# Performance work log

Measured on AMD Instinct MI355X. Metric: run time of the kernel, lower is better.

Reference implementation:

```python
import jax, jax.numpy as jnp
import numpy as np

D_MODEL = 512
N_HEADS = 8
D_K = D_MODEL // N_HEADS
LN_EPS = 1e-5


def setup_inputs() -> dict:
    key = jax.random.key(0)
    ks = jax.random.split(key, 8)
    B, S, D = 2, 4096, D_MODEL
    # xavier_uniform bound for square [D, D] weight
    bound = float(np.sqrt(6.0 / (D + D)))
    x = jax.random.normal(ks[0], (B, S, D), dtype=jnp.float32)
    w_q = jax.random.uniform(ks[1], (D, D), jnp.float32, -bound, bound)
    w_k = jax.random.uniform(ks[2], (D, D), jnp.float32, -bound, bound)
    w_v = jax.random.uniform(ks[3], (D, D), jnp.float32, -bound, bound)
    # w_o: torch Linear default init (kaiming-uniform-ish); uniform is fine as data
    lim = float(1.0 / np.sqrt(D))
    w_o = jax.random.uniform(ks[4], (D, D), jnp.float32, -lim, lim)
    b_o = jax.random.uniform(ks[5], (D,), jnp.float32, -lim, lim)
    ln_gamma = jnp.ones((D,), jnp.float32)
    ln_beta = jnp.zeros((D,), jnp.float32)
    return {"x": x, "w_q": w_q, "w_k": w_k, "w_v": w_v,
            "w_o": w_o, "b_o": b_o, "ln_gamma": ln_gamma, "ln_beta": ln_beta}


def _layer_norm(x, gamma, beta):
    mu = jnp.mean(x, axis=-1, keepdims=True)
    var = jnp.mean(jnp.square(x - mu), axis=-1, keepdims=True)
    return (x - mu) * jax.lax.rsqrt(var + LN_EPS) * gamma + beta


def reference(x, w_q, w_k, w_v, w_o, b_o, ln_gamma, ln_beta):
    B, S, D = x.shape
    residual = x
    h = _layer_norm(x, ln_gamma, ln_beta)
    # torch Linear: y = h @ W.T ; reshape to [B, H, S, d_k]
    def proj(W):
        return (h @ W.T).reshape(B, S, N_HEADS, D_K).transpose(0, 2, 1, 3)
    Q, K, V = proj(w_q), proj(w_k), proj(w_v)
    scores = jnp.einsum('bhqd,bhkd->bhqk', Q, K) / jnp.sqrt(jnp.float32(D_K))
    attn = jax.nn.softmax(scores, axis=-1)  # dropout p=0 -> identity
    attended = jnp.einsum('bhqk,bhkd->bhqd', attn, V)
    attended = attended.transpose(0, 2, 1, 3).reshape(B, S, D)
    out = attended @ w_o.T + b_o
    return out + residual
```

## Files before the change

kernel.cpp:

```cpp
#include <hip/hip_runtime.h>
#include <hip/hip_bf16.h>
#include <stdint.h>


typedef __bf16 bf16;
typedef __attribute__((ext_vector_type(8))) __bf16 bf16x8;
typedef __attribute__((ext_vector_type(4))) __bf16 bf16x4;
typedef __attribute__((ext_vector_type(4))) float f32x4;
typedef __attribute__((ext_vector_type(4))) unsigned int u32x4;

#define LOG2E 1.44269504088896340736f
#define SW(row, grp) (((row) << 6) + ((((grp) ^ ((row) & 7))) << 3))

__device__ __forceinline__ unsigned int pkbf16(float lo, float hi) {
  return __builtin_amdgcn_perm(__builtin_bit_cast(unsigned int, hi),
                               __builtin_bit_cast(unsigned int, lo),
                               0x07060302u);
}

__global__ __launch_bounds__(256) void ln_kernel(
    const float* __restrict__ x, const float* __restrict__ gamma,
    const float* __restrict__ beta, bf16* __restrict__ h) {
  int wave = threadIdx.x >> 6, lane = threadIdx.x & 63;
  int row = blockIdx.x * 4 + wave;
  const float* xr = x + (size_t)row * 512 + lane * 8;
  f32x4 v0 = *(const f32x4*)xr;
  f32x4 v1 = *(const f32x4*)(xr + 4);
  float f[8], s = 0.f, s2 = 0.f;
#pragma unroll
  for (int i = 0; i < 4; ++i) { f[i] = v0[i]; f[4 + i] = v1[i]; }
#pragma unroll
  for (int i = 0; i < 8; ++i) { s += f[i]; s2 += f[i] * f[i]; }
#pragma unroll
  for (int off = 1; off < 64; off <<= 1) {
    s  += __shfl_xor(s, off, 64);
    s2 += __shfl_xor(s2, off, 64);
  }
  float mu  = s * (1.f / 512.f);
  float var = s2 * (1.f / 512.f) - mu * mu;
  float rstd = rsqrtf(var + 1e-5f);
  f32x4 g0 = *(const f32x4*)(gamma + lane * 8);
  f32x4 g1 = *(const f32x4*)(gamma + lane * 8 + 4);
  f32x4 b0 = *(const f32x4*)(beta + lane * 8);
  f32x4 b1 = *(const f32x4*)(beta + lane * 8 + 4);
  bf16x8 o;
#pragma unroll
  for (int i = 0; i < 4; ++i) {
    o[i]     = (bf16)((f[i]     - mu) * rstd * g0[i] + b0[i]);
    o[4 + i] = (bf16)((f[4 + i] - mu) * rstd * g1[i] + b1[i]);
  }
  *(bf16x8*)(h + (size_t)row * 512 + lane * 8) = o;
}

__global__ __launch_bounds__(256) void qkv_kernel(
    const bf16* __restrict__ h, const float* __restrict__ wq,
    const float* __restrict__ wk, const float* __restrict__ wv,
    bf16* __restrict__ Qg, bf16* __restrict__ Kg, bf16* __restrict__ Vtg) {
  __shared__ bf16 As[128 * 64];
  __shared__ bf16 Bs[128 * 64];
  int tid = threadIdx.x, wave = tid >> 6, lane = tid & 63;
  int wm = wave >> 1, wn = wave & 1, quad = lane >> 4, l15 = lane & 15;
  int mtile = blockIdx.x;
  int wsel = blockIdx.y >> 2;
  int nb = blockIdx.y & 3;
  const float* W = (wsel == 0) ? wq : (wsel == 1 ? wk : wv);
  const bf16*  Abase = h + (size_t)mtile * 128 * 512;
  const float* Bbase = W + (size_t)nb * 128 * 512;
  f32x4 acc[4][4];
#pragma unroll
  for (int i = 0; i < 4; ++i)
#pragma unroll
    for (int j = 0; j < 4; ++j) acc[i][j] = (f32x4){0.f, 0.f, 0.f, 0.f};

  int srow = tid >> 3, grp = tid & 7, scol = grp * 8;
  bf16x8 ar[4];
  f32x4 br0[4], br1[4];
#pragma unroll
  for (int k = 0; k < 4; ++k) {
    int rr = srow + k * 32;
    ar[k]  = *(const bf16x8*)(Abase + (size_t)rr * 512 + scol);
    br0[k] = *(const f32x4*)(Bbase + (size_t)rr * 512 + scol);
    br1[k] = *(const f32x4*)(Bbase + (size_t)rr * 512 + scol + 4);
  }
  for (int k0 = 0; k0 < 512; k0 += 64) {
#pragma unroll
    for (int k = 0; k < 4; ++k) {
      int rr = srow + k * 32;
      int w = SW(rr, grp);
      *(bf16x8*)(As + w) = ar[k];
      bf16x8 wb;
#pragma unroll
      for (int j = 0; j < 4; ++j) { wb[j] = (bf16)br0[k][j]; wb[4 + j] = (bf16)br1[k][j]; }
      *(bf16x8*)(Bs + w) = wb;
    }
    __syncthreads();
    if (k0 < 448) {
#pragma unroll
      for (int k = 0; k < 4; ++k) {
        int rr = srow + k * 32;
        ar[k]  = *(const bf16x8*)(Abase + (size_t)rr * 512 + k0 + 64 + scol);
        br0[k] = *(const f32x4*)(Bbase + (size_t)rr * 512 + k0 + 64 + scol);
        br1[k] = *(const f32x4*)(Bbase + (size_t)rr * 512 + k0 + 64 + scol + 4);
      }
    }
#pragma unroll
    for (int c = 0; c < 2; ++c) {
      bf16x8 af[4], bw[4];
#pragma unroll
      for (int mt = 0; mt < 4; ++mt)
        af[mt] = *(const bf16x8*)(As + SW(wm * 64 + mt * 16 + l15, c * 4 + quad));
#pragma unroll
      for (int nt = 0; nt < 4; ++nt)
        bw[nt] = *(const bf16x8*)(Bs + SW(wn * 64 + nt * 16 + l15, c * 4 + quad));
#pragma unroll
      for (int mt = 0; mt < 4; ++mt)
#pragma unroll
        for (int nt = 0; nt < 4; ++nt)
          acc[mt][nt] = __builtin_amdgcn_mfma_f32_16x16x32_bf16(
              bw[nt], af[mt], acc[mt][nt], 0, 0, 0);
    }
    __syncthreads();
  }
  float qscale = (wsel == 0) ? (0.125f * LOG2E) : 1.0f;
#pragma unroll
  for (int mt = 0; mt < 4; ++mt) {
    int m_g = mtile * 128 + wm * 64 + mt * 16 + l15;
    int b = m_g >> 12, s = m_g & 4095;
#pragma unroll
    for (int nt = 0; nt < 4; ++nt) {
      int n_g = nb * 128 + wn * 64 + nt * 16 + quad * 4;
      int head = n_g >> 6, d = n_g & 63;
      f32x4 a = acc[mt][nt];
      if (wsel < 2) {
        bf16* dst = (wsel == 0 ? Qg : Kg) +
                    ((size_t)((b * 8 + head) * 4096 + s)) * 64 + d;
        bf16x4 pk;
#pragma unroll
        for (int r = 0; r < 4; ++r) pk[r] = (bf16)(a[r] * qscale);
        *(bf16x4*)dst = pk;
      } else {
        bf16* dst = Vtg + ((size_t)((b * 8 + head) * 64 + d)) * 4096 + s;
#pragma unroll
        for (int r = 0; r < 4; ++r) dst[(size_t)r * 4096] = (bf16)a[r];
      }
    }
  }
}

__global__ __launch_bounds__(256, 2) void attn_kernel(
    const bf16* __restrict__ Qg, const bf16* __restrict__ Kg,
    const bf16* __restrict__ Vtg, bf16* __restrict__ Og) {
  __shared__ char smem[64 * 1024];
  bf16* KV = (bf16*)smem;
  float* OL = (float*)smem;
  float* Ll = (float*)(smem + 49152);

  int tid = threadIdx.x, wave = tid >> 6, lane = tid & 63;
  int quad = lane >> 4, l15 = lane & 15;
  int qgrp = wave & 1, khalf = wave >> 1;
  int lin = blockIdx.x;
  int bh = ((lin & 7) << 1) | ((lin >> 3) & 1);
  int q0 = (lin >> 4) * 128;
  int hi = bh & 7, bi = bh >> 3;
  const bf16* Kh  = Kg  + (size_t)bh * 4096 * 64;
  const bf16* Vth = Vtg + (size_t)bh * 64 * 4096;

  bf16x8 qf[4][2];
#pragma unroll
  for (int mt = 0; mt < 4; ++mt)
#pragma unroll
    for (int c = 0; c < 2; ++c)
      qf[mt][c] = *(const bf16x8*)(
          Qg + ((size_t)bh * 4096 + q0 + qgrp * 64 + mt * 16 + l15) * 64 +
          c * 32 + quad * 8);

  f32x4 o_acc[4][4], lacc[4];
#pragma unroll
  for (int mt = 0; mt < 4; ++mt) {
    lacc[mt] = (f32x4){0.f, 0.f, 0.f, 0.f};
#pragma unroll
    for (int nt = 0; nt < 4; ++nt) o_acc[mt][nt] = (f32x4){0.f, 0.f, 0.f, 0.f};
  }
  const u32x4 onesu = {0x3F803F80u, 0x3F803F80u, 0x3F803F80u, 0x3F803F80u};
  const bf16x8 ones8 = __builtin_bit_cast(bf16x8, onesu);

  bf16* sbase = KV + khalf * 8192 + (qgrp ? 4096 : 0);
  bf16x8 sr[8];
  int key0 = khalf * 2048;
#pragma unroll
  for (int i = 0; i < 8; ++i) {
    int e = i * 512 + lane * 8;
    sr[i] = qgrp
        ? *(const bf16x8*)(Vth + (size_t)(e >> 6) * 4096 + key0 + (e & 63))
        : *(const bf16x8*)(Kh + (size_t)key0 * 64 + e);
  }
#pragma unroll
  for (int i = 0; i < 8; ++i) {
    int e = i * 512 + lane * 8;
    *(bf16x8*)(sbase + SW(e >> 6, (e >> 3) & 7)) = sr[i];
  }
#pragma unroll
  for (int i = 0; i < 8; ++i) {
    int e = i * 512 + lane * 8;
    sr[i] = qgrp
        ? *(const bf16x8*)(Vth + (size_t)(e >> 6) * 4096 + key0 + 64 + (e & 63))
        : *(const bf16x8*)(Kh + (size_t)(key0 + 64) * 64 + e);
  }
  __syncthreads();

  for (int kt = 0; kt < 32; ++kt) {
    int cur = kt & 1, nxt = cur ^ 1;
    bf16* Ksw = KV + cur * 16384 + khalf * 8192;
    bf16* Vsw = Ksw + 4096;
    if (kt < 31) {
#pragma unroll
      for (int i = 0; i < 8; ++i) {
        int e = i * 512 + lane * 8;
        *(bf16x8*)(sbase + nxt * 16384 + SW(e >> 6, (e >> 3) & 7)) = sr[i];
      }
    }
    if (kt < 30) {
      int kbase = key0 + (kt + 2) * 64;
#pragma unroll
      for (int i = 0; i < 8; ++i) {
        int e = i * 512 + lane * 8;
        sr[i] = qgrp
            ? *(const bf16x8*)(Vth + (size_t)(e >> 6) * 4096 + kbase + (e & 63))
            : *(const bf16x8*)(Kh + (size_t)kbase * 64 + e);
      }
    }
    bf16x8 kf[8];
#pragma unroll
    for (int kb = 0; kb < 4; ++kb)
#pragma unroll
      for (int c = 0; c < 2; ++c)
        kf[kb * 2 + c] = *(const bf16x8*)(Ksw + SW(kb * 16 + l15, c * 4 + quad));
    bf16x8 vf8[2][4];
#pragma unroll
    for (int pr = 0; pr < 2; ++pr)
#pragma unroll
      for (int nt = 0; nt < 4; ++nt) {
        bf16x4 lo = *(const bf16x4*)(
            &Vsw[SW(nt * 16 + l15, (pr * 2) * 2 + (quad >> 1)) + (quad & 1) * 4]);
        bf16x4 hi4 = *(const bf16x4*)(
            &Vsw[SW(nt * 16 + l15, (pr * 2 + 1) * 2 + (quad >> 1)) + (quad & 1) * 4]);
        bf16x8 v;
#pragma unroll
        for (int j = 0; j < 4; ++j) { v[j] = lo[j]; v[4 + j] = hi4[j]; }
        vf8[pr][nt] = v;
      }
#pragma unroll
    for (int mt = 0; mt < 4; ++mt) {
      f32x4 st[4];
#pragma unroll
      for (int kb = 0; kb < 4; ++kb) st[kb] = (f32x4){0.f, 0.f, 0.f, 0.f};
#pragma unroll
      for (int c = 0; c < 2; ++c)
#pragma unroll
        for (int kb = 0; kb < 4; ++kb)
          st[kb] = __builtin_amdgcn_mfma_f32_16x16x32_bf16(
              kf[kb * 2 + c], qf[mt][c], st[kb], 0, 0, 0);
#pragma unroll
      for (int pr = 0; pr < 2; ++pr) {
        float ea[4], eb[4];
#pragma unroll
        for (int r = 0; r < 4; ++r) {
          ea[r] = __builtin_amdgcn_exp2f(st[pr * 2][r]);
          eb[r] = __builtin_amdgcn_exp2f(st[pr * 2 + 1][r]);
        }
        u32x4 pw = {pkbf16(ea[0], ea[1]), pkbf16(ea[2], ea[3]),
                    pkbf16(eb[0], eb[1]), pkbf16(eb[2], eb[3])};
        bf16x8 pk8 = __builtin_bit_cast(bf16x8, pw);
#pragma unroll
        for (int nt = 0; nt < 4; ++nt)
          o_acc[mt][nt] = __builtin_amdgcn_mfma_f32_16x16x32_bf16(
              vf8[pr][nt], pk8, o_acc[mt][nt], 0, 0, 0);
        lacc[mt] = __builtin_amdgcn_mfma_f32_16x16x32_bf16(
            ones8, pk8, lacc[mt], 0, 0, 0);
      }
    }
    __syncthreads();
  }
  if (khalf == 1) {
    float* dst = OL + qgrp * 4096;
#pragma unroll
    for (int mt = 0; mt < 4; ++mt) {
#pragma unroll
      for (int nt = 0; nt < 4; ++nt) {
        int row = mt * 16 + l15;
        int g = nt * 4 + quad;
        int gs = (g & 8) | ((g ^ row) & 7);
        *(f32x4*)(&dst[row * 64 + gs * 4]) = o_acc[mt][nt];
      }
      if (quad == 0) Ll[qgrp * 64 + mt * 16 + l15] = lacc[mt][0];
    }
  }
  __syncthreads();
  if (khalf == 0) {
    const float* src = OL + qgrp * 4096;
#pragma unroll
    for (int mt = 0; mt < 4; ++mt) {
      float lt = lacc[mt][0] + Ll[qgrp * 64 + mt * 16 + l15];
      float inv = 1.0f / lt;
      int q = q0 + qgrp * 64 + mt * 16 + l15;
#pragma unroll
      for (int nt = 0; nt < 4; ++nt) {
        int row = mt * 16 + l15;
        int g = nt * 4 + quad;
        int gs = (g & 8) | ((g ^ row) & 7);
        f32x4 o = *(const f32x4*)(&src[row * 64 + gs * 4]);
        bf16x4 pk;
#pragma unroll
        for (int r = 0; r < 4; ++r)
          pk[r] = (bf16)((o[r] + o_acc[mt][nt][r]) * inv);
        *(bf16x4*)(&Og[((size_t)bi * 4096 + q) * 512 + hi * 64 + nt * 16 +
                       quad * 4]) = pk;
      }
    }
  }
}

__global__ __launch_bounds__(256) void proj_kernel(
    const bf16* __restrict__ A, const float* __restrict__ Wo,
    const float* __restrict__ bo, const float* __restrict__ x,
    float* __restrict__ out) {
  __shared__ bf16 As[128 * 64];
  __shared__ bf16 Bs[128 * 64];
  int tid = threadIdx.x, wave = tid >> 6, lane = tid & 63;
  int wm = wave >> 1, wn = wave & 1, quad = lane >> 4, l15 = lane & 15;
  int mtile = blockIdx.x, nb = blockIdx.y;
  const bf16*  Abase = A + (size_t)mtile * 128 * 512;
  const float* Bbase = Wo + (size_t)nb * 128 * 512;
  f32x4 acc[4][4];
#pragma unroll
  for (int i = 0; i < 4; ++i)
#pragma unroll
    for (int j = 0; j < 4; ++j) acc[i][j] = (f32x4){0.f, 0.f, 0.f, 0.f};

  int srow = tid >> 3, grp = tid & 7, scol = grp * 8;
  bf16x8 ar[4];
  f32x4 br0[4], br1[4];
#pragma unroll
  for (int k = 0; k < 4; ++k) {
    int rr = srow + k * 32;
    ar[k]  = *(const bf16x8*)(Abase + (size_t)rr * 512 + scol);
    br0[k] = *(const f32x4*)(Bbase + (size_t)rr * 512 + scol);
    br1[k] = *(const f32x4*)(Bbase + (size_t)rr * 512 + scol + 4);
  }
  for (int k0 = 0; k0 < 512; k0 += 64) {
#pragma unroll
    for (int k = 0; k < 4; ++k) {
      int rr = srow + k * 32;
      int w = SW(rr, grp);
      *(bf16x8*)(As + w) = ar[k];
      bf16x8 wb;
#pragma unroll
      for (int j = 0; j < 4; ++j) { wb[j] = (bf16)br0[k][j]; wb[4 + j] = (bf16)br1[k][j]; }
      *(bf16x8*)(Bs + w) = wb;
    }
    __syncthreads();
    if (k0 < 448) {
#pragma unroll
      for (int k = 0; k < 4; ++k) {
        int rr = srow + k * 32;
        ar[k]  = *(const bf16x8*)(Abase + (size_t)rr * 512 + k0 + 64 + scol);
        br0[k] = *(const f32x4*)(Bbase + (size_t)rr * 512 + k0 + 64 + scol);
        br1[k] = *(const f32x4*)(Bbase + (size_t)rr * 512 + k0 + 64 + scol + 4);
      }
    }
#pragma unroll
    for (int c = 0; c < 2; ++c) {
      bf16x8 af[4], bw[4];
#pragma unroll
      for (int mt = 0; mt < 4; ++mt)
        af[mt] = *(const bf16x8*)(As + SW(wm * 64 + mt * 16 + l15, c * 4 + quad));
#pragma unroll
      for (int nt = 0; nt < 4; ++nt)
        bw[nt] = *(const bf16x8*)(Bs + SW(wn * 64 + nt * 16 + l15, c * 4 + quad));
#pragma unroll
      for (int mt = 0; mt < 4; ++mt)
#pragma unroll
        for (int nt = 0; nt < 4; ++nt)
          acc[mt][nt] = __builtin_amdgcn_mfma_f32_16x16x32_bf16(
              bw[nt], af[mt], acc[mt][nt], 0, 0, 0);
    }
    __syncthreads();
  }
#pragma unroll
  for (int mt = 0; mt < 4; ++mt) {
    int m_g = mtile * 128 + wm * 64 + mt * 16 + l15;
#pragma unroll
    for (int nt = 0; nt < 4; ++nt) {
      int n_g = nb * 128 + wn * 64 + nt * 16 + quad * 4;
      f32x4 a = acc[mt][nt];
      f32x4 xr = *(const f32x4*)(x + (size_t)m_g * 512 + n_g);
      f32x4 bb = *(const f32x4*)(bo + n_g);
      f32x4 o;
#pragma unroll
      for (int r = 0; r < 4; ++r)
        o[r] = a[r] + bb[r] + xr[r];
      *(f32x4*)(out + (size_t)m_g * 512 + n_g) = o;
    }
  }
}

extern "C" void kernel_launch(void* const* d_in, const int* in_sizes, int n_in,
                              void* d_out, int out_size, void* d_ws, size_t ws_size,
                              hipStream_t stream) {
  const float* x     = (const float*)d_in[0];
  const float* wq    = (const float*)d_in[1];
  const float* wk    = (const float*)d_in[2];
  const float* wv    = (const float*)d_in[3];
  const float* wo    = (const float*)d_in[4];
  const float* bo    = (const float*)d_in[5];
  const float* gamma = (const float*)d_in[6];
  const float* beta  = (const float*)d_in[7];
  float* out = (float*)d_out;
  char* ws = (char*)d_ws;
  const size_t SZ = (size_t)8192 * 512 * sizeof(bf16);
  bf16* h   = (bf16*)(ws);
  bf16* Ao  = (bf16*)(ws);
  bf16* Qg  = (bf16*)(ws + SZ);
  bf16* Kg  = (bf16*)(ws + 2 * SZ);
  bf16* Vtg = (bf16*)(ws + 3 * SZ);

  ln_kernel<<<2048, 256, 0, stream>>>(x, gamma, beta, h);
  qkv_kernel<<<dim3(64, 12), 256, 0, stream>>>(h, wq, wk, wv, Qg, Kg, Vtg);
  attn_kernel<<<512, 256, 0, stream>>>(Qg, Kg, Vtg, Ao);
  proj_kernel<<<dim3(64, 4), 256, 0, stream>>>(Ao, wo, bo, x, out);
}
```

Measured before the change: 191.0 us.

## Pre-convert weights to bf16 in LN kernel and use direct global-to-LDS loads

The LN launch gains extra blocks that convert all four fp32 weight matrices to bf16 in workspace. The QKV and output-projection GEMMs then read bf16 weights instead of converting fp32 per tile, and they stage both tiles with global_load_lds straight into shared memory. This removes the register round-trip and per-tile conversion, but it also drops the register prefetch double-buffering and the XOR swizzle. That likely brings LDS bank conflicts and exposes load latency behind a full waitcnt and barrier each k-step.

```diff
diff --git a/kernel.cpp b/kernel.cpp
--- a/kernel.cpp
+++ b/kernel.cpp
@@ -12,6 +12,12 @@
 #define LOG2E 1.44269504088896340736f
 #define SW(row, grp) (((row) << 6) + ((((grp) ^ ((row) & 7))) << 3))
 
+__device__ __forceinline__ void gl2lds16(const void* g, void* l) {
+  __builtin_amdgcn_global_load_lds(
+      (__attribute__((address_space(1))) void*)(uintptr_t)g,
+      (__attribute__((address_space(3))) void*)(l), 16, 0, 0);
+}
+
 __device__ __forceinline__ unsigned int pkbf16(float lo, float hi) {
   return __builtin_amdgcn_perm(__builtin_bit_cast(unsigned int, hi),
                                __builtin_bit_cast(unsigned int, lo),
@@ -20,7 +26,23 @@
 
 __global__ __launch_bounds__(256) void ln_kernel(
     const float* __restrict__ x, const float* __restrict__ gamma,
-    const float* __restrict__ beta, bf16* __restrict__ h) {
+    const float* __restrict__ beta, const float* __restrict__ wq,
+    const float* __restrict__ wk, const float* __restrict__ wv,
+    const float* __restrict__ wo, bf16* __restrict__ h,
+    bf16* __restrict__ Wb) {
+  if (blockIdx.x >= 2048) {
+    int base = (blockIdx.x - 2048) * 2048 + threadIdx.x * 8;
+    int w = base >> 18;
+    const float* src = (w == 0) ? wq : (w == 1) ? wk : (w == 2) ? wv : wo;
+    int off = base & 262143;
+    f32x4 a = *(const f32x4*)(src + off);
+    f32x4 b = *(const f32x4*)(src + off + 4);
+    bf16x8 o;
+#pragma unroll
+    for (int i = 0; i < 4; ++i) { o[i] = (bf16)a[i]; o[4 + i] = (bf16)b[i]; }
+    *(bf16x8*)(Wb + base) = o;
+    return;
+  }
   int wave = threadIdx.x >> 6, lane = threadIdx.x & 63;
   int row = blockIdx.x * 4 + wave;
   const float* xr = x + (size_t)row * 512 + lane * 8;
@@ -53,8 +75,7 @@
 }
 
 __global__ __launch_bounds__(256) void qkv_kernel(
-    const bf16* __restrict__ h, const float* __restrict__ wq,
-    const float* __restrict__ wk, const float* __restrict__ wv,
+    const bf16* __restrict__ h, const bf16* __restrict__ Wb,
     bf16* __restrict__ Qg, bf16* __restrict__ Kg, bf16* __restrict__ Vtg) {
   __shared__ bf16 As[128 * 64];
   __shared__ bf16 Bs[128 * 64];
@@ -63,55 +84,35 @@
   int mtile = blockIdx.x;
   int wsel = blockIdx.y >> 2;
   int nb = blockIdx.y & 3;
-  const float* W = (wsel == 0) ? wq : (wsel == 1 ? wk : wv);
-  const bf16*  Abase = h + (size_t)mtile * 128 * 512;
-  const float* Bbase = W + (size_t)nb * 128 * 512;
+  const bf16* Abase = h + (size_t)mtile * 128 * 512;
+  const bf16* Bbase = Wb + (size_t)wsel * 262144 + (size_t)nb * 128 * 512;
   f32x4 acc[4][4];
 #pragma unroll
   for (int i = 0; i < 4; ++i)
 #pragma unroll
     for (int j = 0; j < 4; ++j) acc[i][j] = (f32x4){0.f, 0.f, 0.f, 0.f};
 
-  int srow = tid >> 3, grp = tid & 7, scol = grp * 8;
-  bf16x8 ar[4];
-  f32x4 br0[4], br1[4];
-#pragma unroll
-  for (int k = 0; k < 4; ++k) {
-    int rr = srow + k * 32;
-    ar[k]  = *(const bf16x8*)(Abase + (size_t)rr * 512 + scol);
-    br0[k] = *(const f32x4*)(Bbase + (size_t)rr * 512 + scol);
-    br1[k] = *(const f32x4*)(Bbase + (size_t)rr * 512 + scol + 4);
-  }
+  int gr = lane >> 3, gc = (lane & 7) * 8;
   for (int k0 = 0; k0 < 512; k0 += 64) {
 #pragma unroll
-    for (int k = 0; k < 4; ++k) {
-      int rr = srow + k * 32;
-      int w = SW(rr, grp);
-      *(bf16x8*)(As + w) = ar[k];
-      bf16x8 wb;
-#pragma unroll
-      for (int j = 0; j < 4; ++j) { wb[j] = (bf16)br0[k][j]; wb[4 + j] = (bf16)br1[k][j]; }
-      *(bf16x8*)(Bs + w) = wb;
-    }
+    for (int j = 0; j < 4; ++j) {
+      int r0 = wave * 32 + j * 8;
+      gl2lds16(Abase + (size_t)(r0 + gr) * 512 + k0 + gc, As + r0 * 64);
+      gl2lds16(Bbase + (size_t)(r0 + gr) * 512 + k0 + gc, Bs + r0 * 64);
+    }
+    __builtin_amdgcn_s_waitcnt(0);
     __syncthreads();
-    if (k0 < 448) {
-#pragma unroll
-      for (int k = 0; k < 4; ++k) {
-        int rr = srow + k * 32;
-        ar[k]  = *(const bf16x8*)(Abase + (size_t)rr * 512 + k0 + 64 + scol);
-        br0[k] = *(const f32x4*)(Bbase + (size_t)rr * 512 + k0 + 64 + scol);
-        br1[k] = *(const f32x4*)(Bbase + (size_t)rr * 512 + k0 + 64 + scol + 4);
-      }
-    }
 #pragma unroll
     for (int c = 0; c < 2; ++c) {
       bf16x8 af[4], bw[4];
 #pragma unroll
       for (int mt = 0; mt < 4; ++mt)
-        af[mt] = *(const bf16x8*)(As + SW(wm * 64 + mt * 16 + l15, c * 4 + quad));
+        af[mt] = *(const bf16x8*)(As + (wm * 64 + mt * 16 + l15) * 64 +
+                                  c * 32 + quad * 8);
 #pragma unroll
       for (int nt = 0; nt < 4; ++nt)
-        bw[nt] = *(const bf16x8*)(Bs + SW(wn * 64 + nt * 16 + l15, c * 4 + quad));
+        bw[nt] = *(const bf16x8*)(Bs + (wn * 64 + nt * 16 + l15) * 64 +
+                                  c * 32 + quad * 8);
 #pragma unroll
       for (int mt = 0; mt < 4; ++mt)
 #pragma unroll
@@ -321,7 +322,7 @@
 }
 
 __global__ __launch_bounds__(256) void proj_kernel(
-    const bf16* __restrict__ A, const float* __restrict__ Wo,
+    const bf16* __restrict__ A, const bf16* __restrict__ Wob,
     const float* __restrict__ bo, const float* __restrict__ x,
     float* __restrict__ out) {
   __shared__ bf16 As[128 * 64];
@@ -329,54 +330,35 @@
   int tid = threadIdx.x, wave = tid >> 6, lane = tid & 63;
   int wm = wave >> 1, wn = wave & 1, quad = lane >> 4, l15 = lane & 15;
   int mtile = blockIdx.x, nb = blockIdx.y;
-  const bf16*  Abase = A + (size_t)mtile * 128 * 512;
-  const float* Bbase = Wo + (size_t)nb * 128 * 512;
+  const bf16* Abase = A + (size_t)mtile * 128 * 512;
+  const bf16* Bbase = Wob + (size_t)nb * 128 * 512;
   f32x4 acc[4][4];
 #pragma unroll
   for (int i = 0; i < 4; ++i)
 #pragma unroll
     for (int j = 0; j < 4; ++j) acc[i][j] = (f32x4){0.f, 0.f, 0.f, 0.f};
 
-  int srow = tid >> 3, grp = tid & 7, scol = grp * 8;
-  bf16x8 ar[4];
-  f32x4 br0[4], br1[4];
-#pragma unroll
-  for (int k = 0; k < 4; ++k) {
-    int rr = srow + k * 32;
-    ar[k]  = *(const bf16x8*)(Abase + (size_t)rr * 512 + scol);
-    br0[k] = *(const f32x4*)(Bbase + (size_t)rr * 512 + scol);
-    br1[k] = *(const f32x4*)(Bbase + (size_t)rr * 512 + scol + 4);
-  }
+  int gr = lane >> 3, gc = (lane & 7) * 8;
   for (int k0 = 0; k0 < 512; k0 += 64) {
 #pragma unroll
-    for (int k = 0; k < 4; ++k) {
-      int rr = srow + k * 32;
-      int w = SW(rr, grp);
-      *(bf16x8*)(As + w) = ar[k];
-      bf16x8 wb;
-#pragma unroll
-      for (int j = 0; j < 4; ++j) { wb[j] = (bf16)br0[k][j]; wb[4 + j] = (bf16)br1[k][j]; }
-      *(bf16x8*)(Bs + w) = wb;
-    }
+    for (int j = 0; j < 4; ++j) {
+      int r0 = wave * 32 + j * 8;
+      gl2lds16(Abase + (size_t)(r0 + gr) * 512 + k0 + gc, As + r0 * 64);
+      gl2lds16(Bbase + (size_t)(r0 + gr) * 512 + k0 + gc, Bs + r0 * 64);
+    }
+    __builtin_amdgcn_s_waitcnt(0);
     __syncthreads();
-    if (k0 < 448) {
-#pragma unroll
-      for (int k = 0; k < 4; ++k) {
-        int rr = srow + k * 32;
-        ar[k]  = *(const bf16x8*)(Abase + (size_t)rr * 512 + k0 + 64 + scol);
-        br0[k] = *(const f32x4*)(Bbase + (size_t)rr * 512 + k0 + 64 + scol);
-        br1[k] = *(const f32x4*)(Bbase + (size_t)rr * 512 + k0 + 64 + scol + 4);
-      }
-    }
 #pragma unroll
     for (int c = 0; c < 2; ++c) {
       bf16x8 af[4], bw[4];
 #pragma unroll
       for (int mt = 0; mt < 4; ++mt)
-        af[mt] = *(const bf16x8*)(As + SW(wm * 64 + mt * 16 + l15, c * 4 + quad));
+        af[mt] = *(const bf16x8*)(As + (wm * 64 + mt * 16 + l15) * 64 +
+                                  c * 32 + quad * 8);
 #pragma unroll
       for (int nt = 0; nt < 4; ++nt)
-        bw[nt] = *(const bf16x8*)(Bs + SW(wn * 64 + nt * 16 + l15, c * 4 + quad));
+        bw[nt] = *(const bf16x8*)(Bs + (wn * 64 + nt * 16 + l15) * 64 +
+                                  c * 32 + quad * 8);
 #pragma unroll
       for (int mt = 0; mt < 4; ++mt)
 #pragma unroll
@@ -423,9 +405,10 @@
   bf16* Qg  = (bf16*)(ws + SZ);
   bf16* Kg  = (bf16*)(ws + 2 * SZ);
   bf16* Vtg = (bf16*)(ws + 3 * SZ);
-
-  ln_kernel<<<2048, 256, 0, stream>>>(x, gamma, beta, h);
-  qkv_kernel<<<dim3(64, 12), 256, 0, stream>>>(h, wq, wk, wv, Qg, Kg, Vtg);
+  bf16* Wb  = (bf16*)(ws + 4 * SZ);
+
+  ln_kernel<<<2560, 256, 0, stream>>>(x, gamma, beta, wq, wk, wv, wo, h, Wb);
+  qkv_kernel<<<dim3(64, 12), 256, 0, stream>>>(h, Wb, Qg, Kg, Vtg);
   attn_kernel<<<512, 256, 0, stream>>>(Qg, Kg, Vtg, Ao);
-  proj_kernel<<<dim3(64, 4), 256, 0, stream>>>(Ao, wo, bo, x, out);
-}
+  proj_kernel<<<dim3(64, 4), 256, 0, stream>>>(Ao, Wb + 3 * 262144, bo, x, out);
+}
```

Measured after the change: 198.2 us. 1.04x slower.
